# Kernel tuning notes

Measured on AMD Instinct MI355X. Metric: run time of the kernel, lower is better.

Reference implementation:

```python
import jax, jax.numpy as jnp
import numpy as np

S, B, C = 7, 2, 20
D = C + 5 * B  # 30
LAMBDA_COORD = 5.0
LAMBDA_NOOBJ = 0.5
EPS = 1e-6


def _iou_yolo(b1, b2):
    # b1, b2: [..., 4] boxes in (cx, cy, w, h) 'yolo' format
    b1x1 = b1[..., 0] - b1[..., 2] / 2
    b1y1 = b1[..., 1] - b1[..., 3] / 2
    b1x2 = b1[..., 0] + b1[..., 2] / 2
    b1y2 = b1[..., 1] + b1[..., 3] / 2
    b2x1 = b2[..., 0] - b2[..., 2] / 2
    b2y1 = b2[..., 1] - b2[..., 3] / 2
    b2x2 = b2[..., 0] + b2[..., 2] / 2
    b2y2 = b2[..., 1] + b2[..., 3] / 2
    iw = jnp.clip(jnp.minimum(b1x2, b2x2) - jnp.maximum(b1x1, b2x1), 0.0)
    ih = jnp.clip(jnp.minimum(b1y2, b2y2) - jnp.maximum(b1y1, b2y1), 0.0)
    inter = iw * ih
    a1 = jnp.abs((b1x2 - b1x1) * (b1y2 - b1y1))
    a2 = jnp.abs((b2x2 - b2x1) * (b2y2 - b2y1))
    return inter / (a1 + a2 - inter + EPS)


def setup_inputs() -> dict:
    batch = 16384
    key = jax.random.key(0)
    k1, k2, k3 = jax.random.split(key, 3)
    # true coords / classes in (0.05, 0.95) so sqrt(w), sqrt(h) are well-defined
    y_trues = jax.random.uniform(k1, (batch, S, S, D), dtype=jnp.float32) * 0.9 + 0.05
    conf = (jax.random.uniform(k2, (batch, S, S)) < 0.3).astype(jnp.float32)
    y_trues = y_trues.at[..., 4].set(conf)  # objectness indicator is exactly 0 or 1
    y_preds = jax.random.normal(k3, (batch, S, S, D), dtype=jnp.float32)
    return {"y_trues": y_trues, "y_preds": y_preds}


def reference(y_trues, y_preds):
    yt = y_trues.reshape(-1, S * S, D)
    yp = y_preds.reshape(-1, S * S, D)
    batch = yt.shape[0]

    obj = (yt[..., 4] == 1.0).astype(yt.dtype)   # [N, S*S]
    noobj = 1.0 - obj

    iou1 = _iou_yolo(yt[..., 0:4], yp[..., 0:4])
    iou2 = _iou_yolo(yt[..., 0:4], yp[..., 5:9])
    best1 = iou1 > iou2                           # responsible box selection

    box_hat = jnp.where(best1[..., None], yp[..., 0:4], yp[..., 5:9])
    conf_hat = jnp.where(best1, yp[..., 4], yp[..., 9])        # responsible conf
    other_conf_hat = jnp.where(best1, yp[..., 9], yp[..., 4])  # non-responsible conf

    # xy offset loss
    xy = (yt[..., 0] - box_hat[..., 0]) ** 2 + (yt[..., 1] - box_hat[..., 1]) ** 2
    # wh loss: sqrt(true) vs sqrt(|pred + eps|)
    wh = (jnp.sqrt(yt[..., 2]) - jnp.sqrt(jnp.abs(box_hat[..., 2] + EPS))) ** 2 \
       + (jnp.sqrt(yt[..., 3]) - jnp.sqrt(jnp.abs(box_hat[..., 3] + EPS))) ** 2
    # object confidence loss (true conf == 1 in obj cells)
    obj_conf = (yt[..., 4] - conf_hat) ** 2
    # no-object penalty on the NON-responsible box inside object cells (target 0)
    noobj_in_obj = LAMBDA_NOOBJ * other_conf_hat ** 2
    # no-object penalty on BOTH boxes in cells without objects (true conf == 0)
    noobj_cells = LAMBDA_NOOBJ * ((yt[..., 4] - yp[..., 4]) ** 2
                                  + (yt[..., 4] - yp[..., 9]) ** 2)
    # class loss over C classes
    cls = jnp.sum((yt[..., 10:] - yp[..., 10:]) ** 2, axis=-1)

    per_cell = obj * (LAMBDA_COORD * (xy + wh) + obj_conf + noobj_in_obj + cls) \
             + noobj * noobj_cells
    return jnp.sum(per_cell) / batch
```

## Files before the change

### kernel.cpp

```cpp
#include <hip/hip_runtime.h>


#define SS 49
#define DD 30

__device__ __forceinline__ float cell_loss(const float* __restrict__ yt,
                                           const float* __restrict__ yp) {
    const float LAMBDA_COORD = 5.0f;
    const float LAMBDA_NOOBJ = 0.5f;
    const float EPS = 1e-6f;

    float obj = (yt[4] == 1.0f) ? 1.0f : 0.0f;
    float noobj = 1.0f - obj;

    float tx1 = yt[0] - yt[2] * 0.5f, ty1 = yt[1] - yt[3] * 0.5f;
    float tx2 = yt[0] + yt[2] * 0.5f, ty2 = yt[1] + yt[3] * 0.5f;
    float ta = fabsf((tx2 - tx1) * (ty2 - ty1));

    float ax1 = yp[0] - yp[2] * 0.5f, ay1 = yp[1] - yp[3] * 0.5f;
    float ax2 = yp[0] + yp[2] * 0.5f, ay2 = yp[1] + yp[3] * 0.5f;
    float iw1 = fmaxf(fminf(tx2, ax2) - fmaxf(tx1, ax1), 0.0f);
    float ih1 = fmaxf(fminf(ty2, ay2) - fmaxf(ty1, ay1), 0.0f);
    float inter1 = iw1 * ih1;
    float aa = fabsf((ax2 - ax1) * (ay2 - ay1));
    float iou1 = inter1 / (ta + aa - inter1 + EPS);

    float bx1 = yp[5] - yp[7] * 0.5f, by1 = yp[6] - yp[8] * 0.5f;
    float bx2 = yp[5] + yp[7] * 0.5f, by2 = yp[6] + yp[8] * 0.5f;
    float iw2 = fmaxf(fminf(tx2, bx2) - fmaxf(tx1, bx1), 0.0f);
    float ih2 = fmaxf(fminf(ty2, by2) - fmaxf(ty1, by1), 0.0f);
    float inter2 = iw2 * ih2;
    float ba = fabsf((bx2 - bx1) * (by2 - by1));
    float iou2 = inter2 / (ta + ba - inter2 + EPS);

    bool best1 = iou1 > iou2;
    float bh0 = best1 ? yp[0] : yp[5];
    float bh1 = best1 ? yp[1] : yp[6];
    float bh2 = best1 ? yp[2] : yp[7];
    float bh3 = best1 ? yp[3] : yp[8];
    float conf_hat       = best1 ? yp[4] : yp[9];
    float other_conf_hat = best1 ? yp[9] : yp[4];

    float dx = yt[0] - bh0, dy = yt[1] - bh1;
    float xy = dx * dx + dy * dy;

    float sw = sqrtf(yt[2]) - sqrtf(fabsf(bh2 + EPS));
    float sh = sqrtf(yt[3]) - sqrtf(fabsf(bh3 + EPS));
    float wh = sw * sw + sh * sh;

    float dc = yt[4] - conf_hat;
    float obj_conf = dc * dc;

    float noobj_in_obj = LAMBDA_NOOBJ * other_conf_hat * other_conf_hat;

    float d4 = yt[4] - yp[4];
    float d9 = yt[4] - yp[9];
    float noobj_cells = LAMBDA_NOOBJ * (d4 * d4 + d9 * d9);

    float cls = 0.0f;
#pragma unroll
    for (int k = 10; k < DD; ++k) {
        float d = yt[k] - yp[k];
        cls += d * d;
    }

    return obj * (LAMBDA_COORD * (xy + wh) + obj_conf + noobj_in_obj + cls)
         + noobj * noobj_cells;
}

__global__ __launch_bounds__(256)
void yolo_loss_kernel(const float4* __restrict__ yt4,
                      const float4* __restrict__ yp4,
                      float* __restrict__ out,
                      int npairs, float inv_batch) {
    int pair = blockIdx.x * blockDim.x + threadIdx.x;
    float acc = 0.0f;

    if (pair < npairs) {
        const float4* tb = yt4 + (size_t)pair * 15;
        const float4* pb = yp4 + (size_t)pair * 15;
        float t[60], p[60];
#pragma unroll
        for (int i = 0; i < 15; ++i) {
            float4 v = tb[i];
            t[4 * i + 0] = v.x; t[4 * i + 1] = v.y;
            t[4 * i + 2] = v.z; t[4 * i + 3] = v.w;
        }
#pragma unroll
        for (int i = 0; i < 15; ++i) {
            float4 v = pb[i];
            p[4 * i + 0] = v.x; p[4 * i + 1] = v.y;
            p[4 * i + 2] = v.z; p[4 * i + 3] = v.w;
        }
        acc = cell_loss(t, p) + cell_loss(t + DD, p + DD);
    }

#pragma unroll
    for (int off = 32; off > 0; off >>= 1)
        acc += __shfl_down(acc, off, 64);

    __shared__ float wsum[4];
    int lane = threadIdx.x & 63;
    int wave = threadIdx.x >> 6;
    if (lane == 0) wsum[wave] = acc;
    __syncthreads();
    if (threadIdx.x == 0) {
        float s = wsum[0] + wsum[1] + wsum[2] + wsum[3];
        atomicAdd(out, s * inv_batch);
    }
}

extern "C" void kernel_launch(void* const* d_in, const int* in_sizes, int n_in,
                              void* d_out, int out_size, void* d_ws, size_t ws_size,
                              hipStream_t stream) {
    const float4* yt4 = (const float4*)d_in[0];
    const float4* yp4 = (const float4*)d_in[1];
    float* out = (float*)d_out;

    int total = in_sizes[0];
    int ncells = total / DD;
    int batch = ncells / SS;
    int npairs = ncells / 2;

    hipMemsetAsync(out, 0, sizeof(float), stream);

    int block = 256;
    int grid = (npairs + block - 1) / block;
    yolo_loss_kernel<<<grid, block, 0, stream>>>(yt4, yp4, out, npairs,
                                                 1.0f / (float)batch);
}
```

Before: 213.7 us.

## Stage cell tiles through LDS via async global_load_lds for coalesced loads

Each 128-thread block copies its contiguous tile of y_true and y_pred into LDS with global_load_lds 16-byte async copies that are fully coalesced across the wave, then each thread computes one cell from LDS. This replaces the old scheme of two cells per thread, where each thread did strided float4 loads. The aim is better global access coalescing and lower register pressure. The cost is 30 KB of LDS per block, which can limit occupancy. The grid assumes ncells is a multiple of 128 and has no tail guard.

```diff
diff --git a/kernel.cpp b/kernel.cpp
--- a/kernel.cpp
+++ b/kernel.cpp
@@ -3,30 +3,72 @@
 
 #define SS 49
 #define DD 30
+#define TPB 128
+#define TILE_F (TPB * DD)
+#define TILE_F4 (TILE_F / 4)
+#define NCHUNK 30
 
-__device__ __forceinline__ float cell_loss(const float* __restrict__ yt,
-                                           const float* __restrict__ yp) {
+__device__ __forceinline__ void async_copy16(const float* g, float* l) {
+    __builtin_amdgcn_global_load_lds(
+        (const __attribute__((address_space(1))) void*)g,
+        (__attribute__((address_space(3))) void*)l, 16, 0, 0);
+}
+
+__global__ __launch_bounds__(TPB)
+void yolo_loss_kernel(const float* __restrict__ yt_g,
+                      const float* __restrict__ yp_g,
+                      float* __restrict__ out,
+                      float inv_batch) {
     const float LAMBDA_COORD = 5.0f;
     const float LAMBDA_NOOBJ = 0.5f;
     const float EPS = 1e-6f;
 
-    float obj = (yt[4] == 1.0f) ? 1.0f : 0.0f;
+    __shared__ float smem[2 * TILE_F];
+    __shared__ float wsum[TPB / 64];
+
+    const int tid = threadIdx.x;
+    const int lane = tid & 63;
+    const int wave = tid >> 6;
+    const size_t tile_base = (size_t)blockIdx.x * TILE_F;
+
+    for (int j = wave; j < NCHUNK; j += 2) {
+        const float* g = (j < 15)
+            ? yt_g + tile_base + (size_t)j * 256 + lane * 4
+            : yp_g + tile_base + (size_t)(j - 15) * 256 + lane * 4;
+        async_copy16(g, &smem[j * 256 + lane * 4]);
+    }
+    __builtin_amdgcn_s_waitcnt(0);
+    __syncthreads();
+
+    const float* yt = &smem[tid * DD];
+    const float* yp = &smem[TILE_F + tid * DD];
+
+    float t[DD], p[DD];
+#pragma unroll
+    for (int i = 0; i < DD / 2; ++i) {
+        float2 a = reinterpret_cast<const float2*>(yt)[i];
+        t[2 * i] = a.x; t[2 * i + 1] = a.y;
+        float2 b = reinterpret_cast<const float2*>(yp)[i];
+        p[2 * i] = b.x; p[2 * i + 1] = b.y;
+    }
+
+    float obj = (t[4] == 1.0f) ? 1.0f : 0.0f;
     float noobj = 1.0f - obj;
 
-    float tx1 = yt[0] - yt[2] * 0.5f, ty1 = yt[1] - yt[3] * 0.5f;
-    float tx2 = yt[0] + yt[2] * 0.5f, ty2 = yt[1] + yt[3] * 0.5f;
+    float tx1 = t[0] - t[2] * 0.5f, ty1 = t[1] - t[3] * 0.5f;
+    float tx2 = t[0] + t[2] * 0.5f, ty2 = t[1] + t[3] * 0.5f;
     float ta = fabsf((tx2 - tx1) * (ty2 - ty1));
 
-    float ax1 = yp[0] - yp[2] * 0.5f, ay1 = yp[1] - yp[3] * 0.5f;
-    float ax2 = yp[0] + yp[2] * 0.5f, ay2 = yp[1] + yp[3] * 0.5f;
+    float ax1 = p[0] - p[2] * 0.5f, ay1 = p[1] - p[3] * 0.5f;
+    float ax2 = p[0] + p[2] * 0.5f, ay2 = p[1] + p[3] * 0.5f;
     float iw1 = fmaxf(fminf(tx2, ax2) - fmaxf(tx1, ax1), 0.0f);
     float ih1 = fmaxf(fminf(ty2, ay2) - fmaxf(ty1, ay1), 0.0f);
     float inter1 = iw1 * ih1;
     float aa = fabsf((ax2 - ax1) * (ay2 - ay1));
     float iou1 = inter1 / (ta + aa - inter1 + EPS);
 
-    float bx1 = yp[5] - yp[7] * 0.5f, by1 = yp[6] - yp[8] * 0.5f;
-    float bx2 = yp[5] + yp[7] * 0.5f, by2 = yp[6] + yp[8] * 0.5f;
+    float bx1 = p[5] - p[7] * 0.5f, by1 = p[6] - p[8] * 0.5f;
+    float bx2 = p[5] + p[7] * 0.5f, by2 = p[6] + p[8] * 0.5f;
     float iw2 = fmaxf(fminf(tx2, bx2) - fmaxf(tx1, bx1), 0.0f);
     float ih2 = fmaxf(fminf(ty2, by2) - fmaxf(ty1, by1), 0.0f);
     float inter2 = iw2 * ih2;
@@ -34,98 +76,61 @@
     float iou2 = inter2 / (ta + ba - inter2 + EPS);
 
     bool best1 = iou1 > iou2;
-    float bh0 = best1 ? yp[0] : yp[5];
-    float bh1 = best1 ? yp[1] : yp[6];
-    float bh2 = best1 ? yp[2] : yp[7];
-    float bh3 = best1 ? yp[3] : yp[8];
-    float conf_hat       = best1 ? yp[4] : yp[9];
-    float other_conf_hat = best1 ? yp[9] : yp[4];
+    float bh0 = best1 ? p[0] : p[5];
+    float bh1 = best1 ? p[1] : p[6];
+    float bh2 = best1 ? p[2] : p[7];
+    float bh3 = best1 ? p[3] : p[8];
+    float conf_hat       = best1 ? p[4] : p[9];
+    float other_conf_hat = best1 ? p[9] : p[4];
 
-    float dx = yt[0] - bh0, dy = yt[1] - bh1;
+    float dx = t[0] - bh0, dy = t[1] - bh1;
     float xy = dx * dx + dy * dy;
 
-    float sw = sqrtf(yt[2]) - sqrtf(fabsf(bh2 + EPS));
-    float sh = sqrtf(yt[3]) - sqrtf(fabsf(bh3 + EPS));
+    float sw = sqrtf(t[2]) - sqrtf(fabsf(bh2 + EPS));
+    float sh = sqrtf(t[3]) - sqrtf(fabsf(bh3 + EPS));
     float wh = sw * sw + sh * sh;
 
-    float dc = yt[4] - conf_hat;
+    float dc = t[4] - conf_hat;
     float obj_conf = dc * dc;
 
     float noobj_in_obj = LAMBDA_NOOBJ * other_conf_hat * other_conf_hat;
 
-    float d4 = yt[4] - yp[4];
-    float d9 = yt[4] - yp[9];
+    float d4 = t[4] - p[4];
+    float d9 = t[4] - p[9];
     float noobj_cells = LAMBDA_NOOBJ * (d4 * d4 + d9 * d9);
 
     float cls = 0.0f;
 #pragma unroll
     for (int k = 10; k < DD; ++k) {
-        float d = yt[k] - yp[k];
+        float d = t[k] - p[k];
         cls += d * d;
     }
 
-    return obj * (LAMBDA_COORD * (xy + wh) + obj_conf + noobj_in_obj + cls)
-         + noobj * noobj_cells;
-}
-
-__global__ __launch_bounds__(256)
-void yolo_loss_kernel(const float4* __restrict__ yt4,
-                      const float4* __restrict__ yp4,
-                      float* __restrict__ out,
-                      int npairs, float inv_batch) {
-    int pair = blockIdx.x * blockDim.x + threadIdx.x;
-    float acc = 0.0f;
-
-    if (pair < npairs) {
-        const float4* tb = yt4 + (size_t)pair * 15;
-        const float4* pb = yp4 + (size_t)pair * 15;
-        float t[60], p[60];
-#pragma unroll
-        for (int i = 0; i < 15; ++i) {
-            float4 v = tb[i];
-            t[4 * i + 0] = v.x; t[4 * i + 1] = v.y;
-            t[4 * i + 2] = v.z; t[4 * i + 3] = v.w;
-        }
-#pragma unroll
-        for (int i = 0; i < 15; ++i) {
-            float4 v = pb[i];
-            p[4 * i + 0] = v.x; p[4 * i + 1] = v.y;
-            p[4 * i + 2] = v.z; p[4 * i + 3] = v.w;
-        }
-        acc = cell_loss(t, p) + cell_loss(t + DD, p + DD);
-    }
+    float acc = obj * (LAMBDA_COORD * (xy + wh) + obj_conf + noobj_in_obj + cls)
+              + noobj * noobj_cells;
 
 #pragma unroll
     for (int off = 32; off > 0; off >>= 1)
         acc += __shfl_down(acc, off, 64);
-
-    __shared__ float wsum[4];
-    int lane = threadIdx.x & 63;
-    int wave = threadIdx.x >> 6;
     if (lane == 0) wsum[wave] = acc;
     __syncthreads();
-    if (threadIdx.x == 0) {
-        float s = wsum[0] + wsum[1] + wsum[2] + wsum[3];
-        atomicAdd(out, s * inv_batch);
-    }
+    if (tid == 0)
+        atomicAdd(out, (wsum[0] + wsum[1]) * inv_batch);
 }
 
 extern "C" void kernel_launch(void* const* d_in, const int* in_sizes, int n_in,
                               void* d_out, int out_size, void* d_ws, size_t ws_size,
                               hipStream_t stream) {
-    const float4* yt4 = (const float4*)d_in[0];
-    const float4* yp4 = (const float4*)d_in[1];
+    const float* yt = (const float*)d_in[0];
+    const float* yp = (const float*)d_in[1];
     float* out = (float*)d_out;
 
     int total = in_sizes[0];
     int ncells = total / DD;
     int batch = ncells / SS;
-    int npairs = ncells / 2;
 
     hipMemsetAsync(out, 0, sizeof(float), stream);
 
-    int block = 256;
-    int grid = (npairs + block - 1) / block;
-    yolo_loss_kernel<<<grid, block, 0, stream>>>(yt4, yp4, out, npairs,
-                                                 1.0f / (float)batch);
+    int grid = ncells / TPB;
+    yolo_loss_kernel<<<grid, TPB, 0, stream>>>(yt, yp, out, 1.0f / (float)batch);
 }
```

New measurement: 233.2 us. +9.1%, slower.
